# Kernel tuning notes

Measured on AMD Instinct MI355X. Metric: run time of the kernel, lower is better.

## Reference

```python
import jax, jax.numpy as jnp
import numpy as np

C = 256
C8 = C // 8

def setup_inputs() -> dict:
    key = jax.random.key(0)
    ks = jax.random.split(key, 7)
    B, H, W = 4, 64, 64
    x = jax.random.normal(ks[0], (B, C, H, W), dtype=jnp.float32)
    s = 1.0 / np.sqrt(C)
    Wq = jax.random.normal(ks[1], (C8, C), dtype=jnp.float32) * s
    bq = jnp.zeros((C8,), dtype=jnp.float32)
    Wk = jax.random.normal(ks[2], (C8, C), dtype=jnp.float32) * s
    bk = jnp.zeros((C8,), dtype=jnp.float32)
    Wv = jax.random.normal(ks[3], (C, C), dtype=jnp.float32) * s
    bv = jnp.zeros((C,), dtype=jnp.float32)
    return {"x": x, "Wq": Wq, "bq": bq, "Wk": Wk, "bk": bk, "Wv": Wv, "bv": bv}

def reference(x, Wq, bq, Wk, bk, Wv, bv):
    B, Cc, H, W = x.shape
    xf = x.reshape(B, Cc, H * W)                      # [B, C, N]
    # 1x1 convs == per-pixel linear projections
    q = jnp.einsum('dc,bcn->bdn', Wq, xf) + bq[None, :, None]   # [B, C/8, N]
    k = jnp.einsum('dc,bcn->bdn', Wk, xf) + bk[None, :, None]   # [B, C/8, N]
    v = jnp.einsum('dc,bcn->bdn', Wv, xf) + bv[None, :, None]   # [B, C,   N]
    scores = jnp.einsum('bdi,bdj->bij', q, k)         # [B, N, N] (no scaling, matching source)
    attn = jax.nn.softmax(scores, axis=-1)
    out = jnp.einsum('bcj,bij->bci', v, attn)         # [B, C, N]
    return out.reshape(B, Cc, H, W) + x
```

## Files before the change

kernel.cpp:

```cpp
#include <hip/hip_runtime.h>
#include <math.h>

#define CCH   256
#define NPIX  4096
#define BATCH 4

typedef __attribute__((ext_vector_type(8))) short s16x8;
typedef __attribute__((ext_vector_type(4))) float f32x4;

__device__ __forceinline__ unsigned short f2bf(float f) {
    unsigned int u = __float_as_uint(f);
    u += 0x7fff + ((u >> 16) & 1);
    return (unsigned short)(u >> 16);
}
__device__ __forceinline__ float bf2f(unsigned short h) {
    return __uint_as_float(((unsigned int)h) << 16);
}

__device__ __forceinline__ size_t qk_addr(int b, int n, int d) {
    return ((((size_t)b * 256 + (n >> 4)) * 64 + ((d >> 3) << 4) + (n & 15)) << 3) + (d & 7);
}
__device__ __forceinline__ size_t v_addr(int b, int j, int c) {
    return ((((((size_t)b * 64 + (j >> 6)) * 16 + (c >> 4)) * 2 + ((j >> 5) & 1)) * 64
            + (((j >> 3) & 3) << 4) + (c & 15)) << 3) + (j & 7);
}

__global__ __launch_bounds__(64) void wcast_kernel(
    const float* __restrict__ Wq, const float* __restrict__ bq,
    const float* __restrict__ Wk, const float* __restrict__ bk,
    const float* __restrict__ Wv, const float* __restrict__ bv,
    unsigned short* __restrict__ wfh, unsigned short* __restrict__ wfl,
    float* __restrict__ bias_ws)
{
    const int rt = blockIdx.x;
    const int lane = threadIdx.x, l15 = lane & 15, quad = lane >> 4;
    const float *Ws, *bs; int roff; float scale = 1.0f;
    if (rt < 2)      { Ws = Wq; bs = bq; roff = rt * 16;      scale = 1.44269504f; }
    else if (rt < 4) { Ws = Wk; bs = bk; roff = (rt - 2) * 16; }
    else             { Ws = Wv; bs = bv; roff = (rt - 4) * 16; }

    const float* wrow = Ws + (size_t)(roff + l15) * CCH + quad * 8;
    for (int kb = 0; kb < 8; ++kb) {
        s16x8 h, l;
        #pragma unroll
        for (int d = 0; d < 8; ++d) {
            float wv = wrow[kb * 32 + d] * scale;
            unsigned short hh = f2bf(wv);
            h[d] = (short)hh;
            l[d] = (short)f2bf(wv - bf2f(hh));
        }
        *(s16x8*)&wfh[(((size_t)rt * 8 + kb) * 64 + lane) * 8] = h;
        if (rt < 4) *(s16x8*)&wfl[(((size_t)rt * 8 + kb) * 64 + lane) * 8] = l;
    }
    if (lane < 16) bias_ws[rt * 16 + lane] = bs[roff + lane] * scale;
}

__global__ __launch_bounds__(256, 4) void proj_kernel(
    const float* __restrict__ x,
    const unsigned short* __restrict__ wfh, const unsigned short* __restrict__ wfl,
    const float* __restrict__ bias_ws,
    unsigned short* __restrict__ q_hi, unsigned short* __restrict__ q_lo,
    unsigned short* __restrict__ k_hi, unsigned short* __restrict__ k_lo,
    unsigned short* __restrict__ v_frag)
{
    const int t = threadIdx.x;
    const int rh = t >> 6, lane = t & 63, l15 = lane & 15, quad = lane >> 4;
    const int b = blockIdx.y;
    const int nt = blockIdx.x;

    const float* xb = x + (size_t)b * CCH * NPIX + nt * 16 + l15;
    s16x8 xh[8], xl[8];
    #pragma unroll
    for (int kb = 0; kb < 8; ++kb) {
        s16x8 vh, vl;
        #pragma unroll
        for (int d = 0; d < 8; ++d) {
            float xv = xb[(size_t)(kb * 32 + quad * 8 + d) * NPIX];
            unsigned short h = f2bf(xv);
            vh[d] = (short)h;
            vl[d] = (short)f2bf(xv - bf2f(h));
        }
        xh[kb] = vh; xl[kb] = vl;
    }

    const int n = nt * 16 + l15;
    #pragma unroll 1
    for (int tt = 0; tt < 5; ++tt) {
        const int rt = rh * 5 + tt;
        if (rt < 4) {
            f32x4 acc0 = {0.f, 0.f, 0.f, 0.f};
            f32x4 acc1 = {0.f, 0.f, 0.f, 0.f};
            #pragma unroll
            for (int kb = 0; kb < 8; ++kb) {
                s16x8 ah = *(const s16x8*)&wfh[(((size_t)rt * 8 + kb) * 64 + lane) * 8];
                s16x8 al = *(const s16x8*)&wfl[(((size_t)rt * 8 + kb) * 64 + lane) * 8];
                acc0 = __builtin_amdgcn_mfma_f32_16x16x32_bf16(ah, xh[kb], acc0, 0, 0, 0);
                acc1 = __builtin_amdgcn_mfma_f32_16x16x32_bf16(ah, xl[kb], acc1, 0, 0, 0);
                acc1 = __builtin_amdgcn_mfma_f32_16x16x32_bf16(al, xh[kb], acc1, 0, 0, 0);
            }
            #pragma unroll
            for (int rr = 0; rr < 4; ++rr) {
                const int rloc = quad * 4 + rr;
                const float val = acc0[rr] + acc1[rr] + bias_ws[rt * 16 + rloc];
                unsigned short h = f2bf(val);
                unsigned short l = f2bf(val - bf2f(h));
                if (rt < 2) {
                    const size_t a = qk_addr(b, n, rt * 16 + rloc);
                    q_hi[a] = h; q_lo[a] = l;
                } else {
                    const size_t a = qk_addr(b, n, (rt - 2) * 16 + rloc);
                    k_hi[a] = h; k_lo[a] = l;
                }
            }
        } else {
            f32x4 acc = {0.f, 0.f, 0.f, 0.f};
            #pragma unroll
            for (int kb = 0; kb < 8; ++kb) {
                s16x8 ah = *(const s16x8*)&wfh[(((size_t)rt * 8 + kb) * 64 + lane) * 8];
                acc = __builtin_amdgcn_mfma_f32_16x16x32_bf16(ah, xh[kb], acc, 0, 0, 0);
            }
            #pragma unroll
            for (int rr = 0; rr < 4; ++rr) {
                const int rloc = quad * 4 + rr;
                const float val = acc[rr] + bias_ws[rt * 16 + rloc];
                v_frag[v_addr(b, n, (rt - 4) * 16 + rloc)] = f2bf(val);
            }
        }
    }
}

__global__ __launch_bounds__(512, 4) void attn_kernel(
    const unsigned short* __restrict__ q_hi, const unsigned short* __restrict__ q_lo,
    const unsigned short* __restrict__ k_hi, const unsigned short* __restrict__ k_lo,
    const unsigned short* __restrict__ v_frag,
    const float* __restrict__ x, float* __restrict__ out)
{
    __shared__ unsigned short p_lds[2][2][4][512];
    __shared__ float comb[2][4][64][20];
    __shared__ float lds_l[2][2][16];

    const int t = threadIdx.x;
    const int w = t >> 6, lane = t & 63, l15 = lane & 15, quad = lane >> 4;
    const int jh = w >> 2, ch = w & 3;

    const int f = blockIdx.x;
    const int xcd = f & 7;
    const int b = xcd >> 1;
    const int ib = ((xcd & 1) << 6) + (f >> 3);

    s16x8 qfh0, qfl0, qfh1, qfl1;
    {
        const size_t qo0 = ((size_t)b * 256 + ib * 2 + 0) * 512 + (size_t)lane * 8;
        const size_t qo1 = ((size_t)b * 256 + ib * 2 + 1) * 512 + (size_t)lane * 8;
        qfh0 = *(const s16x8*)(q_hi + qo0);  qfl0 = *(const s16x8*)(q_lo + qo0);
        qfh1 = *(const s16x8*)(q_hi + qo1);  qfl1 = *(const s16x8*)(q_lo + qo1);
    }

    const s16x8 ones = { (short)0x3F80, (short)0x3F80, (short)0x3F80, (short)0x3F80,
                         (short)0x3F80, (short)0x3F80, (short)0x3F80, (short)0x3F80 };

    f32x4 acc[8];
    #pragma unroll
    for (int i = 0; i < 8; ++i) acc[i] = (f32x4){0.f, 0.f, 0.f, 0.f};
    f32x4 lacc = {0.f, 0.f, 0.f, 0.f};

    const unsigned short* khb = k_hi + (size_t)b * 131072 + (size_t)lane * 8;
    const unsigned short* klb = k_lo + (size_t)b * 131072 + (size_t)lane * 8;
    const unsigned short* vb  = v_frag + (size_t)b * 1048576 + (size_t)lane * 8;

    const int prow = ((ch & 1) << 1) + (quad >> 1);
    const int pcol = ((quad & 1) << 2);
    const int pfrag_jj = ch >> 1;

    #pragma unroll 1
    for (int j5 = 0; j5 < 32; ++j5) {
        const int jt = jh * 32 + j5;
        const int buf = j5 & 1;
        const size_t ko = (size_t)(jt * 4 + ch) * 512;
        const s16x8 kfh = *(const s16x8*)(khb + ko);
        const s16x8 kfl = *(const s16x8*)(klb + ko);
        #pragma unroll
        for (int it = 0; it < 2; ++it) {
            f32x4 a0;
            if (it == 0) {
                a0 = __builtin_amdgcn_mfma_f32_16x16x32_bf16(kfh, qfl0, (f32x4){0.f,0.f,0.f,0.f}, 0, 0, 0);
                a0 = __builtin_amdgcn_mfma_f32_16x16x32_bf16(kfl, qfh0, a0, 0, 0, 0);
                a0 = __builtin_amdgcn_mfma_f32_16x16x32_bf16(kfh, qfh0, a0, 0, 0, 0);
            } else {
                a0 = __builtin_amdgcn_mfma_f32_16x16x32_bf16(kfh, qfl1, (f32x4){0.f,0.f,0.f,0.f}, 0, 0, 0);
                a0 = __builtin_amdgcn_mfma_f32_16x16x32_bf16(kfl, qfh1, a0, 0, 0, 0);
                a0 = __builtin_amdgcn_mfma_f32_16x16x32_bf16(kfh, qfh1, a0, 0, 0, 0);
            }
            unsigned int u0 = __float_as_uint(__builtin_exp2f(a0[0])) + 0x8000u;
            unsigned int u1 = __float_as_uint(__builtin_exp2f(a0[1])) + 0x8000u;
            unsigned int u2 = __float_as_uint(__builtin_exp2f(a0[2])) + 0x8000u;
            unsigned int u3 = __float_as_uint(__builtin_exp2f(a0[3])) + 0x8000u;
            uint2 pv;
            pv.x = __builtin_amdgcn_perm(u1, u0, 0x07060302u);
            pv.y = __builtin_amdgcn_perm(u3, u2, 0x07060302u);
            *(uint2*)&p_lds[jh][buf][it * 2 + pfrag_jj][(prow * 16 + l15) * 8 + pcol] = pv;
        }
        __syncthreads();
        const s16x8 pf0 = *(const s16x8*)&p_lds[jh][buf][0][lane * 8];
        const s16x8 pf1 = *(const s16x8*)&p_lds[jh][buf][1][lane * 8];
        const s16x8 pf2 = *(const s16x8*)&p_lds[jh][buf][2][lane * 8];
        const s16x8 pf3 = *(const s16x8*)&p_lds[jh][buf][3][lane * 8];
        if (ch == 0) {
            lacc = __builtin_amdgcn_mfma_f32_16x16x32_bf16(ones, pf0, lacc, 0, 0, 0);
            lacc = __builtin_amdgcn_mfma_f32_16x16x32_bf16(ones, pf1, lacc, 0, 0, 0);
        } else if (ch == 1) {
            lacc = __builtin_amdgcn_mfma_f32_16x16x32_bf16(ones, pf2, lacc, 0, 0, 0);
            lacc = __builtin_amdgcn_mfma_f32_16x16x32_bf16(ones, pf3, lacc, 0, 0, 0);
        }
        #pragma unroll
        for (int ct = 0; ct < 4; ++ct) {
            const size_t vo = (((size_t)jt * 16 + ch * 4 + ct) * 2) * 512;
            const s16x8 v0 = *(const s16x8*)(vb + vo);
            const s16x8 v1 = *(const s16x8*)(vb + vo + 512);
            acc[ct * 2 + 0] = __builtin_amdgcn_mfma_f32_16x16x32_bf16(v0, pf0, acc[ct * 2 + 0], 0, 0, 0);
            acc[ct * 2 + 0] = __builtin_amdgcn_mfma_f32_16x16x32_bf16(v1, pf1, acc[ct * 2 + 0], 0, 0, 0);
            acc[ct * 2 + 1] = __builtin_amdgcn_mfma_f32_16x16x32_bf16(v0, pf2, acc[ct * 2 + 1], 0, 0, 0);
            acc[ct * 2 + 1] = __builtin_amdgcn_mfma_f32_16x16x32_bf16(v1, pf3, acc[ct * 2 + 1], 0, 0, 0);
        }
    }

    if (ch < 2 && lane < 16) lds_l[jh][ch][lane] = lacc[0];
    if (jh == 0) {
        #pragma unroll
        for (int ct = 0; ct < 4; ++ct)
            *(f32x4*)&comb[0][ch][lane][ct * 4] = acc[ct * 2 + 1];
    } else {
        #pragma unroll
        for (int ct = 0; ct < 4; ++ct)
            *(f32x4*)&comb[1][ch][lane][ct * 4] = acc[ct * 2 + 0];
    }
    __syncthreads();
    const float linv = 1.f / (lds_l[0][jh][l15] + lds_l[1][jh][l15]);
    const int ibase = (ib * 2 + jh) * 16 + l15;
    #pragma unroll
    for (int ct = 0; ct < 4; ++ct) {
        f32x4 a;
        if (jh == 0) a = acc[ct * 2 + 0];
        else         a = acc[ct * 2 + 1];
        a += *(const f32x4*)&comb[1 - jh][ch][lane][ct * 4];
        #pragma unroll
        for (int rr = 0; rr < 4; ++rr) {
            const int c = ch * 64 + ct * 16 + quad * 4 + rr;
            const size_t idx = ((size_t)b * CCH + c) * NPIX + ibase;
            out[idx] = a[rr] * linv + x[idx];
        }
    }
}

extern "C" void kernel_launch(void* const* d_in, const int* in_sizes, int n_in,
                              void* d_out, int out_size, void* d_ws, size_t ws_size,
                              hipStream_t stream) {
    const float* x  = (const float*)d_in[0];
    const float* Wq = (const float*)d_in[1];
    const float* bq = (const float*)d_in[2];
    const float* Wk = (const float*)d_in[3];
    const float* bk = (const float*)d_in[4];
    const float* Wv = (const float*)d_in[5];
    const float* bv = (const float*)d_in[6];
    float* out = (float*)d_out;

    unsigned short* ws = (unsigned short*)d_ws;
    unsigned short* q_hi   = ws;
    unsigned short* q_lo   = ws + 524288;
    unsigned short* k_hi   = ws + 1048576;
    unsigned short* k_lo   = ws + 1572864;
    unsigned short* v_frag = ws + 2097152;
    unsigned short* wfh    = ws + 6291456;
    unsigned short* wfl    = ws + 6373376;
    float*          bias_ws = (float*)(ws + 6389760);

    wcast_kernel<<<20, 64, 0, stream>>>(Wq, bq, Wk, bk, Wv, bv, wfh, wfl, bias_ws);
    proj_kernel<<<dim3(256, BATCH), 256, 0, stream>>>(x, wfh, wfl, bias_ws,
                                                      q_hi, q_lo, k_hi, k_lo, v_frag);
    attn_kernel<<<512, 512, 0, stream>>>(q_hi, q_lo, k_hi, k_lo, v_frag, x, out);
}
```

Baseline: 180.3 us.

## Software-pipeline attention score and PV stages and repack projection blocks

The attention loop is software-pipelined. Scores and exp for tile n are computed and written to the alternate LDS buffer while the PV MFMAs consume tile n-1. This leaves one barrier per iteration and lets softmax work overlap matrix work. The row-sum MFMAs are spread across all four channel waves, one each, and the results are combined afterwards. The projection kernel now runs 512-thread blocks covering two pixel tiles, with row tiles interleaved across waves. The cost is extra register pressure from the in-flight tiles and more complex indexing.

```diff
diff --git a/kernel.cpp b/kernel.cpp
--- a/kernel.cpp
+++ b/kernel.cpp
@@ -55,7 +55,7 @@
     if (lane < 16) bias_ws[rt * 16 + lane] = bs[roff + lane] * scale;
 }
 
-__global__ __launch_bounds__(256, 4) void proj_kernel(
+__global__ __launch_bounds__(512, 4) void proj_kernel(
     const float* __restrict__ x,
     const unsigned short* __restrict__ wfh, const unsigned short* __restrict__ wfl,
     const float* __restrict__ bias_ws,
@@ -64,9 +64,10 @@
     unsigned short* __restrict__ v_frag)
 {
     const int t = threadIdx.x;
-    const int rh = t >> 6, lane = t & 63, l15 = lane & 15, quad = lane >> 4;
+    const int w = t >> 6, lane = t & 63, l15 = lane & 15, quad = lane >> 4;
+    const int np = w & 1, rq = w >> 1;
     const int b = blockIdx.y;
-    const int nt = blockIdx.x;
+    const int nt = blockIdx.x * 2 + np;
 
     const float* xb = x + (size_t)b * CCH * NPIX + nt * 16 + l15;
     s16x8 xh[8], xl[8];
@@ -86,7 +87,7 @@
     const int n = nt * 16 + l15;
     #pragma unroll 1
     for (int tt = 0; tt < 5; ++tt) {
-        const int rt = rh * 5 + tt;
+        const int rt = tt * 4 + rq;
         if (rt < 4) {
             f32x4 acc0 = {0.f, 0.f, 0.f, 0.f};
             f32x4 acc1 = {0.f, 0.f, 0.f, 0.f};
@@ -137,7 +138,7 @@
 {
     __shared__ unsigned short p_lds[2][2][4][512];
     __shared__ float comb[2][4][64][20];
-    __shared__ float lds_l[2][2][16];
+    __shared__ float lds_l[2][4][16];
 
     const int t = threadIdx.x;
     const int w = t >> 6, lane = t & 63, l15 = lane & 15, quad = lane >> 4;
@@ -172,10 +173,8 @@
     const int pcol = ((quad & 1) << 2);
     const int pfrag_jj = ch >> 1;
 
-    #pragma unroll 1
-    for (int j5 = 0; j5 < 32; ++j5) {
-        const int jt = jh * 32 + j5;
-        const int buf = j5 & 1;
+    {
+        const int jt = jh * 32;
         const size_t ko = (size_t)(jt * 4 + ch) * 512;
         const s16x8 kfh = *(const s16x8*)(khb + ko);
         const s16x8 kfl = *(const s16x8*)(klb + ko);
@@ -198,33 +197,65 @@
             uint2 pv;
             pv.x = __builtin_amdgcn_perm(u1, u0, 0x07060302u);
             pv.y = __builtin_amdgcn_perm(u3, u2, 0x07060302u);
-            *(uint2*)&p_lds[jh][buf][it * 2 + pfrag_jj][(prow * 16 + l15) * 8 + pcol] = pv;
-        }
+            *(uint2*)&p_lds[jh][0][it * 2 + pfrag_jj][(prow * 16 + l15) * 8 + pcol] = pv;
+        }
+    }
+
+    #pragma unroll 1
+    for (int n = 1; n <= 32; ++n) {
         __syncthreads();
-        const s16x8 pf0 = *(const s16x8*)&p_lds[jh][buf][0][lane * 8];
-        const s16x8 pf1 = *(const s16x8*)&p_lds[jh][buf][1][lane * 8];
-        const s16x8 pf2 = *(const s16x8*)&p_lds[jh][buf][2][lane * 8];
-        const s16x8 pf3 = *(const s16x8*)&p_lds[jh][buf][3][lane * 8];
-        if (ch == 0) {
-            lacc = __builtin_amdgcn_mfma_f32_16x16x32_bf16(ones, pf0, lacc, 0, 0, 0);
-            lacc = __builtin_amdgcn_mfma_f32_16x16x32_bf16(ones, pf1, lacc, 0, 0, 0);
-        } else if (ch == 1) {
-            lacc = __builtin_amdgcn_mfma_f32_16x16x32_bf16(ones, pf2, lacc, 0, 0, 0);
-            lacc = __builtin_amdgcn_mfma_f32_16x16x32_bf16(ones, pf3, lacc, 0, 0, 0);
-        }
-        #pragma unroll
-        for (int ct = 0; ct < 4; ++ct) {
-            const size_t vo = (((size_t)jt * 16 + ch * 4 + ct) * 2) * 512;
-            const s16x8 v0 = *(const s16x8*)(vb + vo);
-            const s16x8 v1 = *(const s16x8*)(vb + vo + 512);
-            acc[ct * 2 + 0] = __builtin_amdgcn_mfma_f32_16x16x32_bf16(v0, pf0, acc[ct * 2 + 0], 0, 0, 0);
-            acc[ct * 2 + 0] = __builtin_amdgcn_mfma_f32_16x16x32_bf16(v1, pf1, acc[ct * 2 + 0], 0, 0, 0);
-            acc[ct * 2 + 1] = __builtin_amdgcn_mfma_f32_16x16x32_bf16(v0, pf2, acc[ct * 2 + 1], 0, 0, 0);
-            acc[ct * 2 + 1] = __builtin_amdgcn_mfma_f32_16x16x32_bf16(v1, pf3, acc[ct * 2 + 1], 0, 0, 0);
-        }
-    }
-
-    if (ch < 2 && lane < 16) lds_l[jh][ch][lane] = lacc[0];
+        const int rb = 1 - (n & 1);
+        const s16x8 pf0 = *(const s16x8*)&p_lds[jh][rb][0][lane * 8];
+        const s16x8 pf1 = *(const s16x8*)&p_lds[jh][rb][1][lane * 8];
+        const s16x8 pf2 = *(const s16x8*)&p_lds[jh][rb][2][lane * 8];
+        const s16x8 pf3 = *(const s16x8*)&p_lds[jh][rb][3][lane * 8];
+        if (n < 32) {
+            const int jt = jh * 32 + n;
+            const size_t ko = (size_t)(jt * 4 + ch) * 512;
+            const s16x8 kfh = *(const s16x8*)(khb + ko);
+            const s16x8 kfl = *(const s16x8*)(klb + ko);
+            #pragma unroll
+            for (int it = 0; it < 2; ++it) {
+                f32x4 a0;
+                if (it == 0) {
+                    a0 = __builtin_amdgcn_mfma_f32_16x16x32_bf16(kfh, qfl0, (f32x4){0.f,0.f,0.f,0.f}, 0, 0, 0);
+                    a0 = __builtin_amdgcn_mfma_f32_16x16x32_bf16(kfl, qfh0, a0, 0, 0, 0);
+                    a0 = __builtin_amdgcn_mfma_f32_16x16x32_bf16(kfh, qfh0, a0, 0, 0, 0);
+                } else {
+                    a0 = __builtin_amdgcn_mfma_f32_16x16x32_bf16(kfh, qfl1, (f32x4){0.f,0.f,0.f,0.f}, 0, 0, 0);
+                    a0 = __builtin_amdgcn_mfma_f32_16x16x32_bf16(kfl, qfh1, a0, 0, 0, 0);
+                    a0 = __builtin_amdgcn_mfma_f32_16x16x32_bf16(kfh, qfh1, a0, 0, 0, 0);
+                }
+                unsigned int u0 = __float_as_uint(__builtin_exp2f(a0[0])) + 0x8000u;
+                unsigned int u1 = __float_as_uint(__builtin_exp2f(a0[1])) + 0x8000u;
+                unsigned int u2 = __float_as_uint(__builtin_exp2f(a0[2])) + 0x8000u;
+                unsigned int u3 = __float_as_uint(__builtin_exp2f(a0[3])) + 0x8000u;
+                uint2 pv;
+                pv.x = __builtin_amdgcn_perm(u1, u0, 0x07060302u);
+                pv.y = __builtin_amdgcn_perm(u3, u2, 0x07060302u);
+                *(uint2*)&p_lds[jh][n & 1][it * 2 + pfrag_jj][(prow * 16 + l15) * 8 + pcol] = pv;
+            }
+        }
+        if (ch == 0)      lacc = __builtin_amdgcn_mfma_f32_16x16x32_bf16(ones, pf0, lacc, 0, 0, 0);
+        else if (ch == 2) lacc = __builtin_amdgcn_mfma_f32_16x16x32_bf16(ones, pf1, lacc, 0, 0, 0);
+        else if (ch == 1) lacc = __builtin_amdgcn_mfma_f32_16x16x32_bf16(ones, pf2, lacc, 0, 0, 0);
+        else              lacc = __builtin_amdgcn_mfma_f32_16x16x32_bf16(ones, pf3, lacc, 0, 0, 0);
+        {
+            const int jtv = jh * 32 + n - 1;
+            #pragma unroll
+            for (int ct = 0; ct < 4; ++ct) {
+                const size_t vo = (((size_t)jtv * 16 + ch * 4 + ct) * 2) * 512;
+                const s16x8 v0 = *(const s16x8*)(vb + vo);
+                const s16x8 v1 = *(const s16x8*)(vb + vo + 512);
+                acc[ct * 2 + 0] = __builtin_amdgcn_mfma_f32_16x16x32_bf16(v0, pf0, acc[ct * 2 + 0], 0, 0, 0);
+                acc[ct * 2 + 0] = __builtin_amdgcn_mfma_f32_16x16x32_bf16(v1, pf1, acc[ct * 2 + 0], 0, 0, 0);
+                acc[ct * 2 + 1] = __builtin_amdgcn_mfma_f32_16x16x32_bf16(v0, pf2, acc[ct * 2 + 1], 0, 0, 0);
+                acc[ct * 2 + 1] = __builtin_amdgcn_mfma_f32_16x16x32_bf16(v1, pf3, acc[ct * 2 + 1], 0, 0, 0);
+            }
+        }
+    }
+
+    if (lane < 16) lds_l[jh][ch][lane] = lacc[0];
     if (jh == 0) {
         #pragma unroll
         for (int ct = 0; ct < 4; ++ct)
@@ -235,7 +266,10 @@
             *(f32x4*)&comb[1][ch][lane][ct * 4] = acc[ct * 2 + 0];
     }
     __syncthreads();
-    const float linv = 1.f / (lds_l[0][jh][l15] + lds_l[1][jh][l15]);
+    float lsum;
+    if (jh == 0) lsum = (lds_l[0][0][l15] + lds_l[0][2][l15]) + (lds_l[1][0][l15] + lds_l[1][2][l15]);
+    else         lsum = (lds_l[0][1][l15] + lds_l[0][3][l15]) + (lds_l[1][1][l15] + lds_l[1][3][l15]);
+    const float linv = 1.f / lsum;
     const int ibase = (ib * 2 + jh) * 16 + l15;
     #pragma unroll
     for (int ct = 0; ct < 4; ++ct) {
@@ -275,7 +309,7 @@
     float*          bias_ws = (float*)(ws + 6389760);
 
     wcast_kernel<<<20, 64, 0, stream>>>(Wq, bq, Wk, bk, Wv, bv, wfh, wfl, bias_ws);
-    proj_kernel<<<dim3(256, BATCH), 256, 0, stream>>>(x, wfh, wfl, bias_ws,
+    proj_kernel<<<dim3(128, BATCH), 512, 0, stream>>>(x, wfh, wfl, bias_ws,
                                                       q_hi, q_lo, k_hi, k_lo, v_frag);
     attn_kernel<<<512, 512, 0, stream>>>(q_hi, q_lo, k_hi, k_lo, v_frag, x, out);
 }
```

Result: slower. 400.0 us (+121.9%).

## Fuse weight bf16 split into projection kernel and unroll attention loop

Applied to the files above, without the earlier changes.

Removes the separate weight-cast kernel: the projection kernel now reads fp32 weights directly and converts them to bf16 hi/lo fragments inline before each MFMA. The projection block grows to 512 threads covering two pixel tiles, with row tiles interleaved across wave groups. This saves one kernel launch and a workspace round trip, at the cost of redundant per-block weight conversion ALU work. Separately, the attention main loop is unrolled by 2 to give the scheduler more room to overlap work.

```diff
diff --git a/kernel.cpp b/kernel.cpp
--- a/kernel.cpp
+++ b/kernel.cpp
@@ -25,48 +25,20 @@
             + (((j >> 3) & 3) << 4) + (c & 15)) << 3) + (j & 7);
 }
 
-__global__ __launch_bounds__(64) void wcast_kernel(
+__global__ __launch_bounds__(512, 2) void proj_kernel(
+    const float* __restrict__ x,
     const float* __restrict__ Wq, const float* __restrict__ bq,
     const float* __restrict__ Wk, const float* __restrict__ bk,
     const float* __restrict__ Wv, const float* __restrict__ bv,
-    unsigned short* __restrict__ wfh, unsigned short* __restrict__ wfl,
-    float* __restrict__ bias_ws)
-{
-    const int rt = blockIdx.x;
-    const int lane = threadIdx.x, l15 = lane & 15, quad = lane >> 4;
-    const float *Ws, *bs; int roff; float scale = 1.0f;
-    if (rt < 2)      { Ws = Wq; bs = bq; roff = rt * 16;      scale = 1.44269504f; }
-    else if (rt < 4) { Ws = Wk; bs = bk; roff = (rt - 2) * 16; }
-    else             { Ws = Wv; bs = bv; roff = (rt - 4) * 16; }
-
-    const float* wrow = Ws + (size_t)(roff + l15) * CCH + quad * 8;
-    for (int kb = 0; kb < 8; ++kb) {
-        s16x8 h, l;
-        #pragma unroll
-        for (int d = 0; d < 8; ++d) {
-            float wv = wrow[kb * 32 + d] * scale;
-            unsigned short hh = f2bf(wv);
-            h[d] = (short)hh;
-            l[d] = (short)f2bf(wv - bf2f(hh));
-        }
-        *(s16x8*)&wfh[(((size_t)rt * 8 + kb) * 64 + lane) * 8] = h;
-        if (rt < 4) *(s16x8*)&wfl[(((size_t)rt * 8 + kb) * 64 + lane) * 8] = l;
-    }
-    if (lane < 16) bias_ws[rt * 16 + lane] = bs[roff + lane] * scale;
-}
-
-__global__ __launch_bounds__(256, 4) void proj_kernel(
-    const float* __restrict__ x,
-    const unsigned short* __restrict__ wfh, const unsigned short* __restrict__ wfl,
-    const float* __restrict__ bias_ws,
     unsigned short* __restrict__ q_hi, unsigned short* __restrict__ q_lo,
     unsigned short* __restrict__ k_hi, unsigned short* __restrict__ k_lo,
     unsigned short* __restrict__ v_frag)
 {
     const int t = threadIdx.x;
-    const int rh = t >> 6, lane = t & 63, l15 = lane & 15, quad = lane >> 4;
+    const int w = t >> 6, lane = t & 63, l15 = lane & 15, quad = lane >> 4;
+    const int np = w & 1, rq = w >> 1;
     const int b = blockIdx.y;
-    const int nt = blockIdx.x;
+    const int nt = blockIdx.x * 2 + np;
 
     const float* xb = x + (size_t)b * CCH * NPIX + nt * 16 + l15;
     s16x8 xh[8], xl[8];
@@ -86,14 +58,30 @@
     const int n = nt * 16 + l15;
     #pragma unroll 1
     for (int tt = 0; tt < 5; ++tt) {
-        const int rt = rh * 5 + tt;
+        const int rt = tt * 4 + rq;
         if (rt < 4) {
+            const bool isq = (rt < 2);
+            const float scale = isq ? 1.44269504f : 1.0f;
+            const int roff = (isq ? rt : rt - 2) * 16;
+            const float* W  = isq ? Wq : Wk;
+            const float* bs = isq ? bq : bk;
+            const float* wrow = W + (size_t)(roff + l15) * CCH + quad * 8;
             f32x4 acc0 = {0.f, 0.f, 0.f, 0.f};
             f32x4 acc1 = {0.f, 0.f, 0.f, 0.f};
             #pragma unroll
             for (int kb = 0; kb < 8; ++kb) {
-                s16x8 ah = *(const s16x8*)&wfh[(((size_t)rt * 8 + kb) * 64 + lane) * 8];
-                s16x8 al = *(const s16x8*)&wfl[(((size_t)rt * 8 + kb) * 64 + lane) * 8];
+                float4 wa = *(const float4*)(wrow + kb * 32);
+                float4 wb = *(const float4*)(wrow + kb * 32 + 4);
+                s16x8 ah, al;
+                float wv;
+                wv = wa.x * scale; { unsigned short h = f2bf(wv); ah[0] = (short)h; al[0] = (short)f2bf(wv - bf2f(h)); }
+                wv = wa.y * scale; { unsigned short h = f2bf(wv); ah[1] = (short)h; al[1] = (short)f2bf(wv - bf2f(h)); }
+                wv = wa.z * scale; { unsigned short h = f2bf(wv); ah[2] = (short)h; al[2] = (short)f2bf(wv - bf2f(h)); }
+                wv = wa.w * scale; { unsigned short h = f2bf(wv); ah[3] = (short)h; al[3] = (short)f2bf(wv - bf2f(h)); }
+                wv = wb.x * scale; { unsigned short h = f2bf(wv); ah[4] = (short)h; al[4] = (short)f2bf(wv - bf2f(h)); }
+                wv = wb.y * scale; { unsigned short h = f2bf(wv); ah[5] = (short)h; al[5] = (short)f2bf(wv - bf2f(h)); }
+                wv = wb.z * scale; { unsigned short h = f2bf(wv); ah[6] = (short)h; al[6] = (short)f2bf(wv - bf2f(h)); }
+                wv = wb.w * scale; { unsigned short h = f2bf(wv); ah[7] = (short)h; al[7] = (short)f2bf(wv - bf2f(h)); }
                 acc0 = __builtin_amdgcn_mfma_f32_16x16x32_bf16(ah, xh[kb], acc0, 0, 0, 0);
                 acc1 = __builtin_amdgcn_mfma_f32_16x16x32_bf16(ah, xl[kb], acc1, 0, 0, 0);
                 acc1 = __builtin_amdgcn_mfma_f32_16x16x32_bf16(al, xh[kb], acc1, 0, 0, 0);
@@ -101,29 +89,33 @@
             #pragma unroll
             for (int rr = 0; rr < 4; ++rr) {
                 const int rloc = quad * 4 + rr;
-                const float val = acc0[rr] + acc1[rr] + bias_ws[rt * 16 + rloc];
+                const float val = acc0[rr] + acc1[rr] + bs[roff + rloc] * scale;
                 unsigned short h = f2bf(val);
                 unsigned short l = f2bf(val - bf2f(h));
-                if (rt < 2) {
-                    const size_t a = qk_addr(b, n, rt * 16 + rloc);
-                    q_hi[a] = h; q_lo[a] = l;
-                } else {
-                    const size_t a = qk_addr(b, n, (rt - 2) * 16 + rloc);
-                    k_hi[a] = h; k_lo[a] = l;
-                }
+                const size_t a = qk_addr(b, n, roff + rloc);
+                if (isq) { q_hi[a] = h; q_lo[a] = l; }
+                else     { k_hi[a] = h; k_lo[a] = l; }
             }
         } else {
+            const int roff = (rt - 4) * 16;
+            const float* wrow = Wv + (size_t)(roff + l15) * CCH + quad * 8;
             f32x4 acc = {0.f, 0.f, 0.f, 0.f};
             #pragma unroll
             for (int kb = 0; kb < 8; ++kb) {
-                s16x8 ah = *(const s16x8*)&wfh[(((size_t)rt * 8 + kb) * 64 + lane) * 8];
+                float4 wa = *(const float4*)(wrow + kb * 32);
+                float4 wb = *(const float4*)(wrow + kb * 32 + 4);
+                s16x8 ah;
+                ah[0] = (short)f2bf(wa.x); ah[1] = (short)f2bf(wa.y);
+                ah[2] = (short)f2bf(wa.z); ah[3] = (short)f2bf(wa.w);
+                ah[4] = (short)f2bf(wb.x); ah[5] = (short)f2bf(wb.y);
+                ah[6] = (short)f2bf(wb.z); ah[7] = (short)f2bf(wb.w);
                 acc = __builtin_amdgcn_mfma_f32_16x16x32_bf16(ah, xh[kb], acc, 0, 0, 0);
             }
             #pragma unroll
             for (int rr = 0; rr < 4; ++rr) {
                 const int rloc = quad * 4 + rr;
-                const float val = acc[rr] + bias_ws[rt * 16 + rloc];
-                v_frag[v_addr(b, n, (rt - 4) * 16 + rloc)] = f2bf(val);
+                const float val = acc[rr] + bv[roff + rloc];
+                v_frag[v_addr(b, n, roff + rloc)] = f2bf(val);
             }
         }
     }
@@ -172,7 +164,7 @@
     const int pcol = ((quad & 1) << 2);
     const int pfrag_jj = ch >> 1;
 
-    #pragma unroll 1
+    #pragma unroll 2
     for (int j5 = 0; j5 < 32; ++j5) {
         const int jt = jh * 32 + j5;
         const int buf = j5 & 1;
@@ -270,12 +262,8 @@
     unsigned short* k_hi   = ws + 1048576;
     unsigned short* k_lo   = ws + 1572864;
     unsigned short* v_frag = ws + 2097152;
-    unsigned short* wfh    = ws + 6291456;
-    unsigned short* wfl    = ws + 6373376;
-    float*          bias_ws = (float*)(ws + 6389760);
-
-    wcast_kernel<<<20, 64, 0, stream>>>(Wq, bq, Wk, bk, Wv, bv, wfh, wfl, bias_ws);
-    proj_kernel<<<dim3(256, BATCH), 256, 0, stream>>>(x, wfh, wfl, bias_ws,
+
+    proj_kernel<<<dim3(128, BATCH), 512, 0, stream>>>(x, Wq, bq, Wk, bk, Wv, bv,
                                                       q_hi, q_lo, k_hi, k_lo, v_frag);
     attn_kernel<<<512, 512, 0, stream>>>(q_hi, q_lo, k_hi, k_lo, v_frag, x, out);
 }
```

Result: slower. 199.9 us (+10.9%).

## Double query rows per attention block, prefetch K, restructure projection waves

Applied to the files above, without the earlier changes.

The attention kernel now handles 64 query rows per block instead of 32, so each K and V fragment loaded from memory serves four query tiles rather than two. The grid drops to 256 blocks and the accumulator array doubles to 16 vectors. The next K fragment is now prefetched right after the barrier, and the projection kernel uses 512 threads covering two pixel tiles with an interleaved row-tile assignment. The intent is to cut K/V reload traffic and hide K load latency, at the cost of more registers, lower occupancy (launch bound changed to 2) and fewer blocks to spread across the CUs.

```diff
diff --git a/kernel.cpp b/kernel.cpp
--- a/kernel.cpp
+++ b/kernel.cpp
@@ -55,7 +55,7 @@
     if (lane < 16) bias_ws[rt * 16 + lane] = bs[roff + lane] * scale;
 }
 
-__global__ __launch_bounds__(256, 4) void proj_kernel(
+__global__ __launch_bounds__(512, 4) void proj_kernel(
     const float* __restrict__ x,
     const unsigned short* __restrict__ wfh, const unsigned short* __restrict__ wfl,
     const float* __restrict__ bias_ws,
@@ -64,9 +64,10 @@
     unsigned short* __restrict__ v_frag)
 {
     const int t = threadIdx.x;
-    const int rh = t >> 6, lane = t & 63, l15 = lane & 15, quad = lane >> 4;
+    const int w = t >> 6, lane = t & 63, l15 = lane & 15, quad = lane >> 4;
+    const int np = w & 1, rq = w >> 1;
     const int b = blockIdx.y;
-    const int nt = blockIdx.x;
+    const int nt = blockIdx.x * 2 + np;
 
     const float* xb = x + (size_t)b * CCH * NPIX + nt * 16 + l15;
     s16x8 xh[8], xl[8];
@@ -86,7 +87,7 @@
     const int n = nt * 16 + l15;
     #pragma unroll 1
     for (int tt = 0; tt < 5; ++tt) {
-        const int rt = rh * 5 + tt;
+        const int rt = tt * 4 + rq;
         if (rt < 4) {
             f32x4 acc0 = {0.f, 0.f, 0.f, 0.f};
             f32x4 acc1 = {0.f, 0.f, 0.f, 0.f};
@@ -129,15 +130,15 @@
     }
 }
 
-__global__ __launch_bounds__(512, 4) void attn_kernel(
+__global__ __launch_bounds__(512, 2) void attn_kernel(
     const unsigned short* __restrict__ q_hi, const unsigned short* __restrict__ q_lo,
     const unsigned short* __restrict__ k_hi, const unsigned short* __restrict__ k_lo,
     const unsigned short* __restrict__ v_frag,
     const float* __restrict__ x, float* __restrict__ out)
 {
-    __shared__ unsigned short p_lds[2][2][4][512];
-    __shared__ float comb[2][4][64][20];
-    __shared__ float lds_l[2][2][16];
+    __shared__ unsigned short p_lds[2][2][8][512];
+    __shared__ float comb[2][4][64][36];
+    __shared__ float lds_l[2][4][16];
 
     const int t = threadIdx.x;
     const int w = t >> 6, lane = t & 63, l15 = lane & 15, quad = lane >> 4;
@@ -146,22 +147,26 @@
     const int f = blockIdx.x;
     const int xcd = f & 7;
     const int b = xcd >> 1;
-    const int ib = ((xcd & 1) << 6) + (f >> 3);
-
-    s16x8 qfh0, qfl0, qfh1, qfl1;
+    const int ib = ((xcd & 1) << 5) + (f >> 3);
+
+    s16x8 qfh0, qfl0, qfh1, qfl1, qfh2, qfl2, qfh3, qfl3;
     {
-        const size_t qo0 = ((size_t)b * 256 + ib * 2 + 0) * 512 + (size_t)lane * 8;
-        const size_t qo1 = ((size_t)b * 256 + ib * 2 + 1) * 512 + (size_t)lane * 8;
-        qfh0 = *(const s16x8*)(q_hi + qo0);  qfl0 = *(const s16x8*)(q_lo + qo0);
-        qfh1 = *(const s16x8*)(q_hi + qo1);  qfl1 = *(const s16x8*)(q_lo + qo1);
+        const size_t q0 = ((size_t)b * 256 + ib * 4 + 0) * 512 + (size_t)lane * 8;
+        const size_t q1 = ((size_t)b * 256 + ib * 4 + 1) * 512 + (size_t)lane * 8;
+        const size_t q2 = ((size_t)b * 256 + ib * 4 + 2) * 512 + (size_t)lane * 8;
+        const size_t q3 = ((size_t)b * 256 + ib * 4 + 3) * 512 + (size_t)lane * 8;
+        qfh0 = *(const s16x8*)(q_hi + q0);  qfl0 = *(const s16x8*)(q_lo + q0);
+        qfh1 = *(const s16x8*)(q_hi + q1);  qfl1 = *(const s16x8*)(q_lo + q1);
+        qfh2 = *(const s16x8*)(q_hi + q2);  qfl2 = *(const s16x8*)(q_lo + q2);
+        qfh3 = *(const s16x8*)(q_hi + q3);  qfl3 = *(const s16x8*)(q_lo + q3);
     }
 
     const s16x8 ones = { (short)0x3F80, (short)0x3F80, (short)0x3F80, (short)0x3F80,
                          (short)0x3F80, (short)0x3F80, (short)0x3F80, (short)0x3F80 };
 
-    f32x4 acc[8];
+    f32x4 acc[16];
     #pragma unroll
-    for (int i = 0; i < 8; ++i) acc[i] = (f32x4){0.f, 0.f, 0.f, 0.f};
+    for (int i = 0; i < 16; ++i) acc[i] = (f32x4){0.f, 0.f, 0.f, 0.f};
     f32x4 lacc = {0.f, 0.f, 0.f, 0.f};
 
     const unsigned short* khb = k_hi + (size_t)b * 131072 + (size_t)lane * 8;
@@ -171,26 +176,21 @@
     const int prow = ((ch & 1) << 1) + (quad >> 1);
     const int pcol = ((quad & 1) << 2);
     const int pfrag_jj = ch >> 1;
+
+    s16x8 kfh = *(const s16x8*)(khb + (size_t)((jh * 32) * 4 + ch) * 512);
+    s16x8 kfl = *(const s16x8*)(klb + (size_t)((jh * 32) * 4 + ch) * 512);
 
     #pragma unroll 1
     for (int j5 = 0; j5 < 32; ++j5) {
         const int jt = jh * 32 + j5;
         const int buf = j5 & 1;
-        const size_t ko = (size_t)(jt * 4 + ch) * 512;
-        const s16x8 kfh = *(const s16x8*)(khb + ko);
-        const s16x8 kfl = *(const s16x8*)(klb + ko);
-        #pragma unroll
-        for (int it = 0; it < 2; ++it) {
-            f32x4 a0;
-            if (it == 0) {
-                a0 = __builtin_amdgcn_mfma_f32_16x16x32_bf16(kfh, qfl0, (f32x4){0.f,0.f,0.f,0.f}, 0, 0, 0);
-                a0 = __builtin_amdgcn_mfma_f32_16x16x32_bf16(kfl, qfh0, a0, 0, 0, 0);
-                a0 = __builtin_amdgcn_mfma_f32_16x16x32_bf16(kfh, qfh0, a0, 0, 0, 0);
-            } else {
-                a0 = __builtin_amdgcn_mfma_f32_16x16x32_bf16(kfh, qfl1, (f32x4){0.f,0.f,0.f,0.f}, 0, 0, 0);
-                a0 = __builtin_amdgcn_mfma_f32_16x16x32_bf16(kfl, qfh1, a0, 0, 0, 0);
-                a0 = __builtin_amdgcn_mfma_f32_16x16x32_bf16(kfh, qfh1, a0, 0, 0, 0);
-            }
+        #pragma unroll
+        for (int it = 0; it < 4; ++it) {
+            const s16x8 qh = (it == 0) ? qfh0 : (it == 1) ? qfh1 : (it == 2) ? qfh2 : qfh3;
+            const s16x8 ql = (it == 0) ? qfl0 : (it == 1) ? qfl1 : (it == 2) ? qfl2 : qfl3;
+            f32x4 a0 = __builtin_amdgcn_mfma_f32_16x16x32_bf16(kfh, ql, (f32x4){0.f,0.f,0.f,0.f}, 0, 0, 0);
+            a0 = __builtin_amdgcn_mfma_f32_16x16x32_bf16(kfl, qh, a0, 0, 0, 0);
+            a0 = __builtin_amdgcn_mfma_f32_16x16x32_bf16(kfh, qh, a0, 0, 0, 0);
             unsigned int u0 = __float_as_uint(__builtin_exp2f(a0[0])) + 0x8000u;
             unsigned int u1 = __float_as_uint(__builtin_exp2f(a0[1])) + 0x8000u;
             unsigned int u2 = __float_as_uint(__builtin_exp2f(a0[2])) + 0x8000u;
@@ -201,53 +201,99 @@
             *(uint2*)&p_lds[jh][buf][it * 2 + pfrag_jj][(prow * 16 + l15) * 8 + pcol] = pv;
         }
         __syncthreads();
+        {
+            const size_t kon = (size_t)((jh * 32 + ((j5 + 1) & 31)) * 4 + ch) * 512;
+            kfh = *(const s16x8*)(khb + kon);
+            kfl = *(const s16x8*)(klb + kon);
+        }
         const s16x8 pf0 = *(const s16x8*)&p_lds[jh][buf][0][lane * 8];
         const s16x8 pf1 = *(const s16x8*)&p_lds[jh][buf][1][lane * 8];
         const s16x8 pf2 = *(const s16x8*)&p_lds[jh][buf][2][lane * 8];
         const s16x8 pf3 = *(const s16x8*)&p_lds[jh][buf][3][lane * 8];
+        const s16x8 pf4 = *(const s16x8*)&p_lds[jh][buf][4][lane * 8];
+        const s16x8 pf5 = *(const s16x8*)&p_lds[jh][buf][5][lane * 8];
+        const s16x8 pf6 = *(const s16x8*)&p_lds[jh][buf][6][lane * 8];
+        const s16x8 pf7 = *(const s16x8*)&p_lds[jh][buf][7][lane * 8];
         if (ch == 0) {
             lacc = __builtin_amdgcn_mfma_f32_16x16x32_bf16(ones, pf0, lacc, 0, 0, 0);
             lacc = __builtin_amdgcn_mfma_f32_16x16x32_bf16(ones, pf1, lacc, 0, 0, 0);
         } else if (ch == 1) {
             lacc = __builtin_amdgcn_mfma_f32_16x16x32_bf16(ones, pf2, lacc, 0, 0, 0);
             lacc = __builtin_amdgcn_mfma_f32_16x16x32_bf16(ones, pf3, lacc, 0, 0, 0);
+        } else if (ch == 2) {
+            lacc = __builtin_amdgcn_mfma_f32_16x16x32_bf16(ones, pf4, lacc, 0, 0, 0);
+            lacc = __builtin_amdgcn_mfma_f32_16x16x32_bf16(ones, pf5, lacc, 0, 0, 0);
+        } else {
+            lacc = __builtin_amdgcn_mfma_f32_16x16x32_bf16(ones, pf6, lacc, 0, 0, 0);
+            lacc = __builtin_amdgcn_mfma_f32_16x16x32_bf16(ones, pf7, lacc, 0, 0, 0);
         }
         #pragma unroll
         for (int ct = 0; ct < 4; ++ct) {
             const size_t vo = (((size_t)jt * 16 + ch * 4 + ct) * 2) * 512;
             const s16x8 v0 = *(const s16x8*)(vb + vo);
             const s16x8 v1 = *(const s16x8*)(vb + vo + 512);
-            acc[ct * 2 + 0] = __builtin_amdgcn_mfma_f32_16x16x32_bf16(v0, pf0, acc[ct * 2 + 0], 0, 0, 0);
-            acc[ct * 2 + 0] = __builtin_amdgcn_mfma_f32_16x16x32_bf16(v1, pf1, acc[ct * 2 + 0], 0, 0, 0);
-            acc[ct * 2 + 1] = __builtin_amdgcn_mfma_f32_16x16x32_bf16(v0, pf2, acc[ct * 2 + 1], 0, 0, 0);
-            acc[ct * 2 + 1] = __builtin_amdgcn_mfma_f32_16x16x32_bf16(v1, pf3, acc[ct * 2 + 1], 0, 0, 0);
-        }
-    }
-
-    if (ch < 2 && lane < 16) lds_l[jh][ch][lane] = lacc[0];
+            #pragma unroll
+            for (int it = 0; it < 4; ++it) {
+                const s16x8 pa = (it == 0) ? pf0 : (it == 1) ? pf2 : (it == 2) ? pf4 : pf6;
+                const s16x8 pb = (it == 0) ? pf1 : (it == 1) ? pf3 : (it == 2) ? pf5 : pf7;
+                acc[ct * 4 + it] = __builtin_amdgcn_mfma_f32_16x16x32_bf16(v0, pa, acc[ct * 4 + it], 0, 0, 0);
+                acc[ct * 4 + it] = __builtin_amdgcn_mfma_f32_16x16x32_bf16(v1, pb, acc[ct * 4 + it], 0, 0, 0);
+            }
+        }
+    }
+
+    if (lane < 16) lds_l[jh][ch][lane] = lacc[0];
     if (jh == 0) {
         #pragma unroll
-        for (int ct = 0; ct < 4; ++ct)
-            *(f32x4*)&comb[0][ch][lane][ct * 4] = acc[ct * 2 + 1];
+        for (int ct = 0; ct < 4; ++ct) {
+            *(f32x4*)&comb[0][ch][lane][ct * 8 + 0] = acc[ct * 4 + 2];
+            *(f32x4*)&comb[0][ch][lane][ct * 8 + 4] = acc[ct * 4 + 3];
+        }
     } else {
         #pragma unroll
-        for (int ct = 0; ct < 4; ++ct)
-            *(f32x4*)&comb[1][ch][lane][ct * 4] = acc[ct * 2 + 0];
+        for (int ct = 0; ct < 4; ++ct) {
+            *(f32x4*)&comb[1][ch][lane][ct * 8 + 0] = acc[ct * 4 + 0];
+            *(f32x4*)&comb[1][ch][lane][ct * 8 + 4] = acc[ct * 4 + 1];
+        }
     }
     __syncthreads();
-    const float linv = 1.f / (lds_l[0][jh][l15] + lds_l[1][jh][l15]);
-    const int ibase = (ib * 2 + jh) * 16 + l15;
-    #pragma unroll
-    for (int ct = 0; ct < 4; ++ct) {
-        f32x4 a;
-        if (jh == 0) a = acc[ct * 2 + 0];
-        else         a = acc[ct * 2 + 1];
-        a += *(const f32x4*)&comb[1 - jh][ch][lane][ct * 4];
-        #pragma unroll
-        for (int rr = 0; rr < 4; ++rr) {
-            const int c = ch * 64 + ct * 16 + quad * 4 + rr;
-            const size_t idx = ((size_t)b * CCH + c) * NPIX + ibase;
-            out[idx] = a[rr] * linv + x[idx];
+    if (jh == 0) {
+        const float li0 = 1.f / (lds_l[0][0][l15] + lds_l[1][0][l15]);
+        const float li1 = 1.f / (lds_l[0][1][l15] + lds_l[1][1][l15]);
+        #pragma unroll
+        for (int ct = 0; ct < 4; ++ct) {
+            f32x4 a0 = acc[ct * 4 + 0];
+            f32x4 a1 = acc[ct * 4 + 1];
+            a0 += *(const f32x4*)&comb[1][ch][lane][ct * 8 + 0];
+            a1 += *(const f32x4*)&comb[1][ch][lane][ct * 8 + 4];
+            const int i0 = (ib * 4 + 0) * 16 + l15;
+            const int i1 = (ib * 4 + 1) * 16 + l15;
+            #pragma unroll
+            for (int rr = 0; rr < 4; ++rr) {
+                const int c = ch * 64 + ct * 16 + quad * 4 + rr;
+                const size_t base = ((size_t)b * CCH + c) * NPIX;
+                out[base + i0] = a0[rr] * li0 + x[base + i0];
+                out[base + i1] = a1[rr] * li1 + x[base + i1];
+            }
+        }
+    } else {
+        const float li2 = 1.f / (lds_l[0][2][l15] + lds_l[1][2][l15]);
+        const float li3 = 1.f / (lds_l[0][3][l15] + lds_l[1][3][l15]);
+        #pragma unroll
+        for (int ct = 0; ct < 4; ++ct) {
+            f32x4 a2 = acc[ct * 4 + 2];
+            f32x4 a3 = acc[ct * 4 + 3];
+            a2 += *(const f32x4*)&comb[0][ch][lane][ct * 8 + 0];
+            a3 += *(const f32x4*)&comb[0][ch][lane][ct * 8 + 4];
+            const int i2 = (ib * 4 + 2) * 16 + l15;
+            const int i3 = (ib * 4 + 3) * 16 + l15;
+            #pragma unroll
+            for (int rr = 0; rr < 4; ++rr) {
+                const int c = ch * 64 + ct * 16 + quad * 4 + rr;
+                const size_t base = ((size_t)b * CCH + c) * NPIX;
+                out[base + i2] = a2[rr] * li2 + x[base + i2];
+                out[base + i3] = a3[rr] * li3 + x[base + i3];
+            }
         }
     }
 }
@@ -275,7 +321,7 @@
     float*          bias_ws = (float*)(ws + 6389760);
 
     wcast_kernel<<<20, 64, 0, stream>>>(Wq, bq, Wk, bk, Wv, bv, wfh, wfl, bias_ws);
-    proj_kernel<<<dim3(256, BATCH), 256, 0, stream>>>(x, wfh, wfl, bias_ws,
+    proj_kernel<<<dim3(128, BATCH), 512, 0, stream>>>(x, wfh, wfl, bias_ws,
                                                       q_hi, q_lo, k_hi, k_lo, v_frag);
-    attn_kernel<<<512, 512, 0, stream>>>(q_hi, q_lo, k_hi, k_lo, v_frag, x, out);
-}
+    attn_kernel<<<256, 512, 0, stream>>>(q_hi, q_lo, k_hi, k_lo, v_frag, x, out);
+}
```

Result: slower. 186.4 us (+3.4%).
